# Performance work log

Measured on AMD Instinct MI355X. Metric: run time of the kernel, lower is better.

## Reference

```python
import jax, jax.numpy as jnp
import numpy as np

N_NODES, BATCH, VOCAB, HID, OUT = 2047, 128, 32, 128, 128


def setup_inputs() -> dict:
    key = jax.random.key(0)
    ks = jax.random.split(key, 18)
    w = 0.05  # small init scale (xavier-ish for these sizes)
    rn = lambda k, s, sc=w: jax.random.normal(k, s, dtype=jnp.float32) * sc
    return {
        "targets": jax.random.normal(ks[0], (N_NODES, BATCH, VOCAB), dtype=jnp.float32),
        "masks": jnp.ones((N_NODES, BATCH), dtype=jnp.float32),
        "wir_w": rn(ks[1], (HID, VOCAB)), "wir_b": rn(ks[2], (HID,)),
        "whr_w": rn(ks[3], (HID, 2 * HID)), "whr_b": rn(ks[4], (HID,)),
        "wiz_w": rn(ks[5], (HID, VOCAB)), "wiz_b": rn(ks[6], (HID,)),
        "whz_w": rn(ks[7], (HID, 2 * HID)), "whz_b": rn(ks[8], (HID,)),
        "win_w": rn(ks[9], (HID, VOCAB)), "win_b": rn(ks[10], (HID,)),
        "whn_w": rn(ks[11], (HID, 2 * HID)), "whn_b": rn(ks[12], (HID,)),
        "mu_w": rn(ks[13], (OUT, HID)), "mu_b": rn(ks[14], (OUT,)),
        "lv_w": rn(ks[15], (OUT, HID)), "lv_b": rn(ks[16], (OUT,)),
    }


def _encode(targets, masks, wir_w, wir_b, whr_w, whr_b, wiz_w, wiz_b,
            whz_w, whz_b, win_w, win_b, whn_w, whn_b):
    # Complete binary tree in heap layout: level d occupies nodes [2^d-1, 2^(d+1)-1).
    # Bottom-up level sweep == the original node-by-node recursion, but each
    # level's GRU221 cells are batched into one fused GEMM group.
    Nn, B, V = targets.shape
    H = wir_w.shape[0]
    D = int(np.log2(Nn + 1))  # static at trace time
    h_prev = None  # hidden states of the level below, [2^(d+1)*B, H]
    for d in range(D - 1, -1, -1):
        n = 1 << d
        start = n - 1
        x = targets[start:start + n].reshape(n * B, V)
        m = masks[start:start + n].reshape(n * B, 1)
        if h_prev is None:  # leaves: zero children
            h1 = jnp.zeros((n * B, H), dtype=targets.dtype)
            h2 = h1
        else:
            hp = h_prev.reshape(2 * n, B, H)
            h1 = hp[0::2].reshape(n * B, H)  # left children (heap idx 2i+1)
            h2 = hp[1::2].reshape(n * B, H)  # right children (heap idx 2i+2)
        h = jnp.concatenate([h1, h2], axis=1)  # [nB, 2H]
        r = jax.nn.sigmoid(x @ wir_w.T + wir_b + h @ whr_w.T + whr_b)
        z = jax.nn.sigmoid(x @ wiz_w.T + wiz_b + h @ whz_w.T + whz_b)
        c = jnp.tanh(x @ win_w.T + win_b + r * (h @ whn_w.T + whn_b))
        h_out = (1 - z) * c + z * 0.5 * h1 + z * 0.5 * h2
        h_prev = h_out * m
    return h_prev  # root hidden, [B, H]


def reference(targets, masks, wir_w, wir_b, whr_w, whr_b, wiz_w, wiz_b,
              whz_w, whz_b, win_w, win_b, whn_w, whn_b,
              mu_w, mu_b, lv_w, lv_b):
    root = _encode(targets, masks, wir_w, wir_b, whr_w, whr_b,
                   wiz_w, wiz_b, whz_w, whz_b, win_w, win_b, whn_w, whn_b)
    mu = root @ mu_w.T + mu_b
    logvar = root @ lv_w.T + lv_b
    return mu, logvar
```

## Files before the change

kernel.cpp:

```cpp
#include <hip/hip_runtime.h>
#include <hip/hip_bf16.h>
#include <math.h>

#define B 128
#define V 32
#define H 128
#define LDH 264
#define NTHR 256

typedef __attribute__((ext_vector_type(8))) short bf16x8;
typedef __attribute__((ext_vector_type(4))) float f32x4;

__device__ inline f32x4 mfma_wx(bf16x8 wf, bf16x8 xf, f32x4 c) {
    return __builtin_amdgcn_mfma_f32_16x16x32_bf16(wf, xf, c, 0, 0, 0);
}
__device__ inline unsigned short f2bf(float f) {
    __hip_bfloat16 h = __float2bfloat16(f);
    return __builtin_bit_cast(unsigned short, h);
}
__device__ inline float bf2f(unsigned short u) {
    unsigned int x = ((unsigned int)u) << 16;
    return __builtin_bit_cast(float, x);
}
__device__ inline float sig_pre(float y) {
    return __builtin_amdgcn_rcpf(1.f + __builtin_amdgcn_exp2f(y));
}
__device__ inline float tanh_pre(float y) {
    return 1.f - 2.f * __builtin_amdgcn_rcpf(__builtin_amdgcn_exp2f(y) + 1.f);
}
__device__ inline bf16x8 load_xfrag(const float* p) {
    float4 a = *(const float4*)p;
    float4 b = *(const float4*)(p + 4);
    bf16x8 r;
    r[0] = (short)f2bf(a.x); r[1] = (short)f2bf(a.y);
    r[2] = (short)f2bf(a.z); r[3] = (short)f2bf(a.w);
    r[4] = (short)f2bf(b.x); r[5] = (short)f2bf(b.y);
    r[6] = (short)f2bf(b.z); r[7] = (short)f2bf(b.w);
    return r;
}
__device__ inline uint2 pack4(float a, float b, float c, float d) {
    uint2 r;
    r.x = (unsigned int)f2bf(a) | ((unsigned int)f2bf(b) << 16);
    r.y = (unsigned int)f2bf(c) | ((unsigned int)f2bf(d) << 16);
    return r;
}

__global__ void prep_pack(const float* __restrict__ wir_w, const float* __restrict__ whr_w,
                          const float* __restrict__ wiz_w, const float* __restrict__ whz_w,
                          const float* __restrict__ win_w, const float* __restrict__ whn_w,
                          const float* __restrict__ wir_b, const float* __restrict__ whr_b,
                          const float* __restrict__ wiz_b, const float* __restrict__ whz_b,
                          const float* __restrict__ win_b, const float* __restrict__ whn_b,
                          const float* __restrict__ mu_w, const float* __restrict__ mu_b,
                          const float* __restrict__ lv_w, const float* __restrict__ lv_b,
                          unsigned short* __restrict__ wFrag, unsigned short* __restrict__ pFrag,
                          float* __restrict__ bias)
{
    int idx = blockIdx.x * blockDim.x + threadIdx.x;
    if (idx < 13824) {
        int lane = idx & 63;
        int ctks = idx >> 6;
        int ct = ctks % 24;
        int ks = ctks / 24;
        int g = ct >> 3;
        int t = ct & 7;
        int u = t * 16 + (lane & 15);
        const float scl = (g == 2) ? 2.88539008f : -1.44269504f;
        const float* wi = (g == 0) ? wir_w : (g == 1) ? wiz_w : win_w;
        const float* wh = (g == 0) ? whr_w : (g == 1) ? whz_w : whn_w;
        unsigned short v[8] __attribute__((aligned(16)));
        #pragma unroll
        for (int i = 0; i < 8; ++i) {
            float f;
            if (ks == 0) { int k = 8 * (lane >> 4) + i; f = wi[u * V + k]; }
            else         { int k = (ks - 1) * 32 + 8 * (lane >> 4) + i; f = wh[u * 256 + k]; }
            v[i] = f2bf(f * scl);
        }
        *(int4*)(wFrag + (size_t)idx * 8) = *(const int4*)v;
    } else if (idx < 13824 + 4096) {
        int pidx = idx - 13824;
        int lane = pidx & 63;
        int rest = pidx >> 6;
        int ct2 = rest & 15;
        int ks = rest >> 4;
        int sel = ct2 >> 3, tl = ct2 & 7;
        int u = tl * 16 + (lane & 15);
        const float* wsrc = sel ? lv_w : mu_w;
        unsigned short v[8] __attribute__((aligned(16)));
        #pragma unroll
        for (int i = 0; i < 8; ++i) {
            int k = ks * 32 + 8 * (lane >> 4) + i;
            v[i] = f2bf(wsrc[u * H + k]);
        }
        *(int4*)(pFrag + (size_t)pidx * 8) = *(const int4*)v;
    }
    if (idx < 6 * H) {
        int s = idx / H, u = idx % H;
        float val;
        if (s == 0)      val = (wir_b[u] + whr_b[u]) * -1.44269504f;
        else if (s == 1) val = (wiz_b[u] + whz_b[u]) * -1.44269504f;
        else if (s == 2) val = win_b[u] * 2.88539008f;
        else if (s == 3) val = whn_b[u] * 2.88539008f;
        else if (s == 4) val = mu_b[u];
        else             val = lv_b[u];
        bias[idx] = val;
    }
}

__global__ __launch_bounds__(NTHR, 4) void leaf_d9_kernel(
    const float* __restrict__ targets, const float* __restrict__ masks,
    unsigned short* __restrict__ lvl9,
    const unsigned short* __restrict__ wFrag, const float* __restrict__ bias)
{
    __shared__ __attribute__((aligned(16))) unsigned short h_lds[32 * LDH];

    const int tid = threadIdx.x;
    const int lane = tid & 63;
    const int w = tid >> 6;
    const int l15 = lane & 15;
    const int lg = lane >> 4;
    const int j = blockIdx.x >> 2;
    const int q = blockIdx.x & 3;

    bf16x8 w0[2][3];
    #pragma unroll
    for (int t = 0; t < 2; ++t)
        #pragma unroll
        for (int g = 0; g < 3; ++g)
            w0[t][g] = *(const bf16x8*)(wFrag + (((size_t)g * 8 + 2 * w + t) * 64 + lane) * 8);

    f32x4 b_r[2], b_z[2], b_in[2], b_hn[2];
    #pragma unroll
    for (int t = 0; t < 2; ++t) {
        int u0 = w * 32 + t * 16 + lg * 4;
        b_r[t]  = *(const f32x4*)(bias + u0);
        b_z[t]  = *(const f32x4*)(bias + 128 + u0);
        b_in[t] = *(const f32x4*)(bias + 256 + u0);
        b_hn[t] = *(const f32x4*)(bias + 384 + u0);
    }

    const size_t r9 = (size_t)(511 + j) * B + (size_t)q * 32;
    bf16x8 x9_0 = load_xfrag(targets + (r9 + l15) * V + 8 * lg);
    bf16x8 x9_1 = load_xfrag(targets + (r9 + 16 + l15) * V + 8 * lg);

    #pragma unroll
    for (int c = 0; c < 2; ++c) {
        const size_t crow = (size_t)(1023 + 2 * j + c) * B + (size_t)q * 32;
        bf16x8 xf0 = load_xfrag(targets + (crow + l15) * V + 8 * lg);
        bf16x8 xf1 = load_xfrag(targets + (crow + 16 + l15) * V + 8 * lg);
        f32x4 ar[2][2], az[2][2], an[2][2];
        #pragma unroll
        for (int t = 0; t < 2; ++t) {
            ar[0][t] = b_r[t];  ar[1][t] = b_r[t];
            az[0][t] = b_z[t];  az[1][t] = b_z[t];
            an[0][t] = b_in[t]; an[1][t] = b_in[t];
        }
        #pragma unroll
        for (int t = 0; t < 2; ++t) {
            ar[0][t] = mfma_wx(w0[t][0], xf0, ar[0][t]);
            ar[1][t] = mfma_wx(w0[t][0], xf1, ar[1][t]);
            az[0][t] = mfma_wx(w0[t][1], xf0, az[0][t]);
            az[1][t] = mfma_wx(w0[t][1], xf1, az[1][t]);
            an[0][t] = mfma_wx(w0[t][2], xf0, an[0][t]);
            an[1][t] = mfma_wx(w0[t][2], xf1, an[1][t]);
        }
        #pragma unroll
        for (int rt = 0; rt < 2; ++rt) {
            int row = rt * 16 + l15;
            float m = masks[crow + row];
            #pragma unroll
            for (int t = 0; t < 2; ++t) {
                int u0 = w * 32 + t * 16 + lg * 4;
                float ho[4];
                #pragma unroll
                for (int reg = 0; reg < 4; ++reg) {
                    float rg = sig_pre(ar[rt][t][reg]);
                    float zg = sig_pre(az[rt][t][reg]);
                    float cg = tanh_pre(an[rt][t][reg] + rg * b_hn[t][reg]);
                    ho[reg] = (cg - zg * cg) * m;
                }
                *(uint2*)(&h_lds[row * LDH + c * 128 + u0]) = pack4(ho[0], ho[1], ho[2], ho[3]);
            }
        }
    }
    __syncthreads();

    f32x4 acc_r[2][2], acc_z[2][2], acc_in[2][2], acc_hn[2][2];
    #pragma unroll
    for (int t = 0; t < 2; ++t) {
        acc_r[0][t] = b_r[t];   acc_r[1][t] = b_r[t];
        acc_z[0][t] = b_z[t];   acc_z[1][t] = b_z[t];
        acc_in[0][t] = b_in[t]; acc_in[1][t] = b_in[t];
        acc_hn[0][t] = b_hn[t]; acc_hn[1][t] = b_hn[t];
    }
    #pragma unroll
    for (int t = 0; t < 2; ++t) {
        acc_r[0][t] = mfma_wx(w0[t][0], x9_0, acc_r[0][t]);
        acc_r[1][t] = mfma_wx(w0[t][0], x9_1, acc_r[1][t]);
        acc_z[0][t] = mfma_wx(w0[t][1], x9_0, acc_z[0][t]);
        acc_z[1][t] = mfma_wx(w0[t][1], x9_1, acc_z[1][t]);
        acc_in[0][t] = mfma_wx(w0[t][2], x9_0, acc_in[0][t]);
        acc_in[1][t] = mfma_wx(w0[t][2], x9_1, acc_in[1][t]);
    }
    #pragma unroll 2
    for (int ks = 1; ks <= 8; ++ks) {
        bf16x8 a0 = *(const bf16x8*)(&h_lds[l15 * LDH + (ks - 1) * 32 + 8 * lg]);
        bf16x8 a1 = *(const bf16x8*)(&h_lds[(16 + l15) * LDH + (ks - 1) * 32 + 8 * lg]);
        size_t fb = (size_t)ks * 24 * 64;
        #pragma unroll
        for (int t = 0; t < 2; ++t) {
            int tt = 2 * w + t;
            bf16x8 wr_ = *(const bf16x8*)(wFrag + (fb + (size_t)(tt) * 64 + lane) * 8);
            bf16x8 wz_ = *(const bf16x8*)(wFrag + (fb + (size_t)(8 + tt) * 64 + lane) * 8);
            bf16x8 wn_ = *(const bf16x8*)(wFrag + (fb + (size_t)(16 + tt) * 64 + lane) * 8);
            acc_r[0][t] = mfma_wx(wr_, a0, acc_r[0][t]);
            acc_r[1][t] = mfma_wx(wr_, a1, acc_r[1][t]);
            acc_z[0][t] = mfma_wx(wz_, a0, acc_z[0][t]);
            acc_z[1][t] = mfma_wx(wz_, a1, acc_z[1][t]);
            acc_hn[0][t] = mfma_wx(wn_, a0, acc_hn[0][t]);
            acc_hn[1][t] = mfma_wx(wn_, a1, acc_hn[1][t]);
        }
    }
    #pragma unroll
    for (int rt = 0; rt < 2; ++rt) {
        int row = rt * 16 + l15;
        float m = masks[r9 + row];
        #pragma unroll
        for (int t = 0; t < 2; ++t) {
            int u0 = w * 32 + t * 16 + lg * 4;
            ushort4 h1v = *(const ushort4*)(&h_lds[row * LDH + u0]);
            ushort4 h2v = *(const ushort4*)(&h_lds[row * LDH + 128 + u0]);
            const unsigned short* h1p = (const unsigned short*)&h1v;
            const unsigned short* h2p = (const unsigned short*)&h2v;
            float ho[4];
            #pragma unroll
            for (int reg = 0; reg < 4; ++reg) {
                float rg = sig_pre(acc_r[rt][t][reg]);
                float zg = sig_pre(acc_z[rt][t][reg]);
                float cg = tanh_pre(acc_in[rt][t][reg] + rg * acc_hn[rt][t][reg]);
                float hm = 0.5f * bf2f(h1p[reg]) + 0.5f * bf2f(h2p[reg]);
                ho[reg] = (cg + zg * (hm - cg)) * m;
            }
            *(uint2*)(lvl9 + ((size_t)j * B + (size_t)q * 32 + row) * H + u0) =
                pack4(ho[0], ho[1], ho[2], ho[3]);
        }
    }
}

__global__ __launch_bounds__(NTHR, 4) void level_kernel(
    const float* __restrict__ targets, const float* __restrict__ masks,
    int start,
    const unsigned short* __restrict__ prev, unsigned short* __restrict__ outb,
    const unsigned short* __restrict__ wFrag, const float* __restrict__ bias)
{
    __shared__ __attribute__((aligned(16))) unsigned short h_lds[32 * LDH];

    const int tid = threadIdx.x;
    const int lane = tid & 63;
    const int w = tid >> 6;
    const int l15 = lane & 15;
    const int lg = lane >> 4;
    const int n = blockIdx.x >> 2;
    const int q = blockIdx.x & 3;

    #pragma unroll
    for (int t = 0; t < 4; ++t) {
        int task = t * NTHR + tid;
        int row = task >> 5;
        int ck = task & 31;
        int4 v = *(const int4*)(prev + (((size_t)(2 * n + (ck >> 4))) * B + (size_t)q * 32 + row) * H + (ck & 15) * 8);
        *(int4*)(&h_lds[row * LDH + ck * 8]) = v;
    }
    const size_t rx = (size_t)(start + n) * B + (size_t)q * 32;
    bf16x8 x0 = load_xfrag(targets + (rx + l15) * V + 8 * lg);
    bf16x8 x1 = load_xfrag(targets + (rx + 16 + l15) * V + 8 * lg);

    f32x4 b_r[2], b_z[2], b_in[2], b_hn[2];
    #pragma unroll
    for (int t = 0; t < 2; ++t) {
        int u0 = w * 32 + t * 16 + lg * 4;
        b_r[t]  = *(const f32x4*)(bias + u0);
        b_z[t]  = *(const f32x4*)(bias + 128 + u0);
        b_in[t] = *(const f32x4*)(bias + 256 + u0);
        b_hn[t] = *(const f32x4*)(bias + 384 + u0);
    }
    __syncthreads();

    f32x4 acc_r[2][2], acc_z[2][2], acc_in[2][2], acc_hn[2][2];
    #pragma unroll
    for (int t = 0; t < 2; ++t) {
        acc_r[0][t] = b_r[t];   acc_r[1][t] = b_r[t];
        acc_z[0][t] = b_z[t];   acc_z[1][t] = b_z[t];
        acc_in[0][t] = b_in[t]; acc_in[1][t] = b_in[t];
        acc_hn[0][t] = b_hn[t]; acc_hn[1][t] = b_hn[t];
    }
    #pragma unroll
    for (int t = 0; t < 2; ++t) {
        int tt = 2 * w + t;
        bf16x8 wr_ = *(const bf16x8*)(wFrag + ((size_t)(tt) * 64 + lane) * 8);
        bf16x8 wz_ = *(const bf16x8*)(wFrag + ((size_t)(8 + tt) * 64 + lane) * 8);
        bf16x8 wn_ = *(const bf16x8*)(wFrag + ((size_t)(16 + tt) * 64 + lane) * 8);
        acc_r[0][t] = mfma_wx(wr_, x0, acc_r[0][t]);
        acc_r[1][t] = mfma_wx(wr_, x1, acc_r[1][t]);
        acc_z[0][t] = mfma_wx(wz_, x0, acc_z[0][t]);
        acc_z[1][t] = mfma_wx(wz_, x1, acc_z[1][t]);
        acc_in[0][t] = mfma_wx(wn_, x0, acc_in[0][t]);
        acc_in[1][t] = mfma_wx(wn_, x1, acc_in[1][t]);
    }
    #pragma unroll 2
    for (int ks = 1; ks <= 8; ++ks) {
        bf16x8 a0 = *(const bf16x8*)(&h_lds[l15 * LDH + (ks - 1) * 32 + 8 * lg]);
        bf16x8 a1 = *(const bf16x8*)(&h_lds[(16 + l15) * LDH + (ks - 1) * 32 + 8 * lg]);
        size_t fb = (size_t)ks * 24 * 64;
        #pragma unroll
        for (int t = 0; t < 2; ++t) {
            int tt = 2 * w + t;
            bf16x8 wr_ = *(const bf16x8*)(wFrag + (fb + (size_t)(tt) * 64 + lane) * 8);
            bf16x8 wz_ = *(const bf16x8*)(wFrag + (fb + (size_t)(8 + tt) * 64 + lane) * 8);
            bf16x8 wn_ = *(const bf16x8*)(wFrag + (fb + (size_t)(16 + tt) * 64 + lane) * 8);
            acc_r[0][t] = mfma_wx(wr_, a0, acc_r[0][t]);
            acc_r[1][t] = mfma_wx(wr_, a1, acc_r[1][t]);
            acc_z[0][t] = mfma_wx(wz_, a0, acc_z[0][t]);
            acc_z[1][t] = mfma_wx(wz_, a1, acc_z[1][t]);
            acc_hn[0][t] = mfma_wx(wn_, a0, acc_hn[0][t]);
            acc_hn[1][t] = mfma_wx(wn_, a1, acc_hn[1][t]);
        }
    }
    #pragma unroll
    for (int rt = 0; rt < 2; ++rt) {
        int row = rt * 16 + l15;
        float m = masks[rx + row];
        #pragma unroll
        for (int t = 0; t < 2; ++t) {
            int u0 = w * 32 + t * 16 + lg * 4;
            ushort4 h1v = *(const ushort4*)(&h_lds[row * LDH + u0]);
            ushort4 h2v = *(const ushort4*)(&h_lds[row * LDH + 128 + u0]);
            const unsigned short* h1p = (const unsigned short*)&h1v;
            const unsigned short* h2p = (const unsigned short*)&h2v;
            float ho[4];
            #pragma unroll
            for (int reg = 0; reg < 4; ++reg) {
                float rg = sig_pre(acc_r[rt][t][reg]);
                float zg = sig_pre(acc_z[rt][t][reg]);
                float cg = tanh_pre(acc_in[rt][t][reg] + rg * acc_hn[rt][t][reg]);
                float hm = 0.5f * bf2f(h1p[reg]) + 0.5f * bf2f(h2p[reg]);
                ho[reg] = (cg + zg * (hm - cg)) * m;
            }
            *(uint2*)(outb + ((size_t)n * B + (size_t)q * 32 + row) * H + u0) =
                pack4(ho[0], ho[1], ho[2], ho[3]);
        }
    }
}

__global__ __launch_bounds__(NTHR, 4) void pair_kernel(
    const float* __restrict__ targets, const float* __restrict__ masks,
    int du,
    const unsigned short* __restrict__ prev,
    unsigned short* __restrict__ outl,
    const unsigned short* __restrict__ wFrag, const float* __restrict__ bias,
    int do_proj, const unsigned short* __restrict__ pFrag, float* __restrict__ proj_out)
{
    __shared__ __attribute__((aligned(16))) unsigned short hc[32 * LDH];
    __shared__ __attribute__((aligned(16))) unsigned short hp[16 * LDH];

    const int tid = threadIdx.x;
    const int lane = tid & 63;
    const int w = tid >> 6;
    const int l15 = lane & 15;
    const int lg = lane >> 4;
    const int p = blockIdx.x >> 3;
    const int c8 = blockIdx.x & 7;
    const int dl = du - 1;

    #pragma unroll
    for (int t = 0; t < 4; ++t) {
        int task = t * NTHR + tid;
        int row = task >> 5;
        int ck = task & 31;
        int gnode = 4 * p + ((row >> 4) << 1) + (ck >> 4);
        int4 v = *(const int4*)(prev + (((size_t)gnode) * B + (size_t)c8 * 16 + (row & 15)) * H + (ck & 15) * 8);
        *(int4*)(&hc[row * LDH + ck * 8]) = v;
    }
    const size_t cbase = (size_t)((1 << du) - 1) + 2 * p;
    bf16x8 xc0 = load_xfrag(targets + ((cbase) * B + (size_t)c8 * 16 + l15) * V + 8 * lg);
    bf16x8 xc1 = load_xfrag(targets + ((cbase + 1) * B + (size_t)c8 * 16 + l15) * V + 8 * lg);
    const size_t pnode = (size_t)((1 << dl) - 1) + p;
    bf16x8 xp = load_xfrag(targets + (pnode * B + (size_t)c8 * 16 + l15) * V + 8 * lg);

    f32x4 b_r[2], b_z[2], b_in[2], b_hn[2];
    #pragma unroll
    for (int t = 0; t < 2; ++t) {
        int u0 = w * 32 + t * 16 + lg * 4;
        b_r[t]  = *(const f32x4*)(bias + u0);
        b_z[t]  = *(const f32x4*)(bias + 128 + u0);
        b_in[t] = *(const f32x4*)(bias + 256 + u0);
        b_hn[t] = *(const f32x4*)(bias + 384 + u0);
    }
    __syncthreads();

    {
        f32x4 acc_r[2][2], acc_z[2][2], acc_in[2][2], acc_hn[2][2];
        #pragma unroll
        for (int t = 0; t < 2; ++t) {
            acc_r[0][t] = b_r[t];   acc_r[1][t] = b_r[t];
            acc_z[0][t] = b_z[t];   acc_z[1][t] = b_z[t];
            acc_in[0][t] = b_in[t]; acc_in[1][t] = b_in[t];
            acc_hn[0][t] = b_hn[t]; acc_hn[1][t] = b_hn[t];
        }
        #pragma unroll
        for (int t = 0; t < 2; ++t) {
            int tt = 2 * w + t;
            bf16x8 wr_ = *(const bf16x8*)(wFrag + ((size_t)(tt) * 64 + lane) * 8);
            bf16x8 wz_ = *(const bf16x8*)(wFrag + ((size_t)(8 + tt) * 64 + lane) * 8);
            bf16x8 wn_ = *(const bf16x8*)(wFrag + ((size_t)(16 + tt) * 64 + lane) * 8);
            acc_r[0][t] = mfma_wx(wr_, xc0, acc_r[0][t]);
            acc_r[1][t] = mfma_wx(wr_, xc1, acc_r[1][t]);
            acc_z[0][t] = mfma_wx(wz_, xc0, acc_z[0][t]);
            acc_z[1][t] = mfma_wx(wz_, xc1, acc_z[1][t]);
            acc_in[0][t] = mfma_wx(wn_, xc0, acc_in[0][t]);
            acc_in[1][t] = mfma_wx(wn_, xc1, acc_in[1][t]);
        }
        #pragma unroll 2
        for (int ks = 1; ks <= 8; ++ks) {
            bf16x8 a0 = *(const bf16x8*)(&hc[l15 * LDH + (ks - 1) * 32 + 8 * lg]);
            bf16x8 a1 = *(const bf16x8*)(&hc[(16 + l15) * LDH + (ks - 1) * 32 + 8 * lg]);
            size_t fb = (size_t)ks * 24 * 64;
            #pragma unroll
            for (int t = 0; t < 2; ++t) {
                int tt = 2 * w + t;
                bf16x8 wr_ = *(const bf16x8*)(wFrag + (fb + (size_t)(tt) * 64 + lane) * 8);
                bf16x8 wz_ = *(const bf16x8*)(wFrag + (fb + (size_t)(8 + tt) * 64 + lane) * 8);
                bf16x8 wn_ = *(const bf16x8*)(wFrag + (fb + (size_t)(16 + tt) * 64 + lane) * 8);
                acc_r[0][t] = mfma_wx(wr_, a0, acc_r[0][t]);
                acc_r[1][t] = mfma_wx(wr_, a1, acc_r[1][t]);
                acc_z[0][t] = mfma_wx(wz_, a0, acc_z[0][t]);
                acc_z[1][t] = mfma_wx(wz_, a1, acc_z[1][t]);
                acc_hn[0][t] = mfma_wx(wn_, a0, acc_hn[0][t]);
                acc_hn[1][t] = mfma_wx(wn_, a1, acc_hn[1][t]);
            }
        }
        #pragma unroll
        for (int rt = 0; rt < 2; ++rt) {
            float m = masks[(cbase + rt) * B + (size_t)c8 * 16 + l15];
            int hrow = rt * 16 + l15;
            #pragma unroll
            for (int t = 0; t < 2; ++t) {
                int u0 = w * 32 + t * 16 + lg * 4;
                ushort4 h1v = *(const ushort4*)(&hc[hrow * LDH + u0]);
                ushort4 h2v = *(const ushort4*)(&hc[hrow * LDH + 128 + u0]);
                const unsigned short* h1p = (const unsigned short*)&h1v;
                const unsigned short* h2p = (const unsigned short*)&h2v;
                float ho[4];
                #pragma unroll
                for (int reg = 0; reg < 4; ++reg) {
                    float rg = sig_pre(acc_r[rt][t][reg]);
                    float zg = sig_pre(acc_z[rt][t][reg]);
                    float cg = tanh_pre(acc_in[rt][t][reg] + rg * acc_hn[rt][t][reg]);
                    float hm = 0.5f * bf2f(h1p[reg]) + 0.5f * bf2f(h2p[reg]);
                    ho[reg] = (cg + zg * (hm - cg)) * m;
                }
                *(uint2*)(&hp[l15 * LDH + rt * 128 + u0]) = pack4(ho[0], ho[1], ho[2], ho[3]);
            }
        }
    }
    __syncthreads();

    {
        f32x4 acc_r[2], acc_z[2], acc_in[2], acc_hn[2];
        #pragma unroll
        for (int t = 0; t < 2; ++t) {
            acc_r[t] = b_r[t]; acc_z[t] = b_z[t]; acc_in[t] = b_in[t]; acc_hn[t] = b_hn[t];
        }
        #pragma unroll
        for (int t = 0; t < 2; ++t) {
            int tt = 2 * w + t;
            bf16x8 wr_ = *(const bf16x8*)(wFrag + ((size_t)(tt) * 64 + lane) * 8);
            bf16x8 wz_ = *(const bf16x8*)(wFrag + ((size_t)(8 + tt) * 64 + lane) * 8);
            bf16x8 wn_ = *(const bf16x8*)(wFrag + ((size_t)(16 + tt) * 64 + lane) * 8);
            acc_r[t] = mfma_wx(wr_, xp, acc_r[t]);
            acc_z[t] = mfma_wx(wz_, xp, acc_z[t]);
            acc_in[t] = mfma_wx(wn_, xp, acc_in[t]);
        }
        #pragma unroll 2
        for (int ks = 1; ks <= 8; ++ks) {
            bf16x8 a = *(const bf16x8*)(&hp[l15 * LDH + (ks - 1) * 32 + 8 * lg]);
            size_t fb = (size_t)ks * 24 * 64;
            #pragma unroll
            for (int t = 0; t < 2; ++t) {
                int tt = 2 * w + t;
                bf16x8 wr_ = *(const bf16x8*)(wFrag + (fb + (size_t)(tt) * 64 + lane) * 8);
                bf16x8 wz_ = *(const bf16x8*)(wFrag + (fb + (size_t)(8 + tt) * 64 + lane) * 8);
                bf16x8 wn_ = *(const bf16x8*)(wFrag + (fb + (size_t)(16 + tt) * 64 + lane) * 8);
                acc_r[t] = mfma_wx(wr_, a, acc_r[t]);
                acc_z[t] = mfma_wx(wz_, a, acc_z[t]);
                acc_hn[t] = mfma_wx(wn_, a, acc_hn[t]);
            }
        }
        float m = masks[pnode * B + (size_t)c8 * 16 + l15];
        #pragma unroll
        for (int t = 0; t < 2; ++t) {
            int u0 = w * 32 + t * 16 + lg * 4;
            ushort4 h1v = *(const ushort4*)(&hp[l15 * LDH + u0]);
            ushort4 h2v = *(const ushort4*)(&hp[l15 * LDH + 128 + u0]);
            const unsigned short* h1p = (const unsigned short*)&h1v;
            const unsigned short* h2p = (const unsigned short*)&h2v;
            float ho[4];
            #pragma unroll
            for (int reg = 0; reg < 4; ++reg) {
                float rg = sig_pre(acc_r[t][reg]);
                float zg = sig_pre(acc_z[t][reg]);
                float cg = tanh_pre(acc_in[t][reg] + rg * acc_hn[t][reg]);
                float hm = 0.5f * bf2f(h1p[reg]) + 0.5f * bf2f(h2p[reg]);
                ho[reg] = (cg + zg * (hm - cg)) * m;
            }
            uint2 pk = pack4(ho[0], ho[1], ho[2], ho[3]);
            *(uint2*)(outl + ((size_t)p * B + (size_t)c8 * 16 + l15) * H + u0) = pk;
            if (do_proj) *(uint2*)(&hp[l15 * LDH + u0]) = pk;
        }
    }

    if (do_proj) {
        __syncthreads();
        f32x4 pa[4];
        #pragma unroll
        for (int jj = 0; jj < 4; ++jj) {
            int ct2 = 4 * w + jj;
            int sel = ct2 >> 3, tl = ct2 & 7;
            pa[jj] = *(const f32x4*)(bias + 512 + sel * 128 + tl * 16 + lg * 4);
        }
        #pragma unroll
        for (int ks = 0; ks < 4; ++ks) {
            bf16x8 a = *(const bf16x8*)(&hp[l15 * LDH + ks * 32 + 8 * lg]);
            #pragma unroll
            for (int jj = 0; jj < 4; ++jj) {
                bf16x8 f = *(const bf16x8*)(pFrag + (((size_t)ks * 16 + 4 * w + jj) * 64 + lane) * 8);
                pa[jj] = mfma_wx(f, a, pa[jj]);
            }
        }
        #pragma unroll
        for (int jj = 0; jj < 4; ++jj) {
            int ct2 = 4 * w + jj;
            int sel = ct2 >> 3, tl = ct2 & 7;
            int u0 = tl * 16 + lg * 4;
            int row = c8 * 16 + l15;
            *(f32x4*)(proj_out + ((size_t)sel * B + row) * H + u0) = pa[jj];
        }
    }
}

extern "C" void kernel_launch(void* const* d_in, const int* in_sizes, int n_in,
                              void* d_out, int out_size, void* d_ws, size_t ws_size,
                              hipStream_t stream)
{
    const float* targets = (const float*)d_in[0];
    const float* masks   = (const float*)d_in[1];
    const float* wir_w = (const float*)d_in[2];  const float* wir_b = (const float*)d_in[3];
    const float* whr_w = (const float*)d_in[4];  const float* whr_b = (const float*)d_in[5];
    const float* wiz_w = (const float*)d_in[6];  const float* wiz_b = (const float*)d_in[7];
    const float* whz_w = (const float*)d_in[8];  const float* whz_b = (const float*)d_in[9];
    const float* win_w = (const float*)d_in[10]; const float* win_b = (const float*)d_in[11];
    const float* whn_w = (const float*)d_in[12]; const float* whn_b = (const float*)d_in[13];
    const float* mu_w  = (const float*)d_in[14]; const float* mu_b  = (const float*)d_in[15];
    const float* lv_w  = (const float*)d_in[16]; const float* lv_b  = (const float*)d_in[17];

    unsigned short* ws16 = (unsigned short*)d_ws;
    unsigned short* lvl9 = ws16;
    unsigned short* lvl8 = lvl9 + (size_t)512 * B * H;
    unsigned short* lvl6 = lvl8 + (size_t)256 * B * H;
    unsigned short* lvl4 = lvl6 + (size_t)64 * B * H;
    unsigned short* lvl2 = lvl4 + (size_t)16 * B * H;
    unsigned short* lvl0 = lvl2 + (size_t)4 * B * H;
    unsigned short* wFrag = lvl0 + (size_t)1 * B * H;
    unsigned short* pFrag = wFrag + 110592;
    float*          biasw = (float*)(pFrag + 32768);

    prep_pack<<<70, 256, 0, stream>>>(
        wir_w, whr_w, wiz_w, whz_w, win_w, whn_w,
        wir_b, whr_b, wiz_b, whz_b, win_b, whn_b,
        mu_w, mu_b, lv_w, lv_b, wFrag, pFrag, biasw);

    leaf_d9_kernel<<<2048, NTHR, 0, stream>>>(targets, masks, lvl9, wFrag, biasw);

    level_kernel<<<1024, NTHR, 0, stream>>>(targets, masks, 255, lvl9, lvl8, wFrag, biasw);

    pair_kernel<<<512, NTHR, 0, stream>>>(targets, masks, 7, lvl8, lvl6, wFrag, biasw,
                                          0, nullptr, nullptr);
    pair_kernel<<<128, NTHR, 0, stream>>>(targets, masks, 5, lvl6, lvl4, wFrag, biasw,
                                          0, nullptr, nullptr);
    pair_kernel<<<32, NTHR, 0, stream>>>(targets, masks, 3, lvl4, lvl2, wFrag, biasw,
                                         0, nullptr, nullptr);
    pair_kernel<<<8, NTHR, 0, stream>>>(targets, masks, 1, lvl2, lvl0, wFrag, biasw,
                                        1, pFrag, (float*)d_out);
}
```

Before: 136.1 us.

## Fuse leaf, level-9 and level-8 GRU cells into one subtree kernel

Merges the leaf/level-9 kernel and the level-8 kernel into a single kernel in which each block computes two level-9 nodes (each from its two leaf children) and then their level-8 parent. Level-9 hidden states stay in a second LDS buffer instead of going through global memory, which removes one launch and the write and reread of the level-9 activations. In exchange there are half as many blocks, each doing serialized work with extra barriers, and the larger LDS footprint may cut occupancy.

New measurement: 178.8 us. +31.3%, slower.

```diff
diff --git a/kernel.cpp b/kernel.cpp
--- a/kernel.cpp
+++ b/kernel.cpp
@@ -22,12 +22,8 @@
     unsigned int x = ((unsigned int)u) << 16;
     return __builtin_bit_cast(float, x);
 }
-__device__ inline float sig_pre(float y) {
-    return __builtin_amdgcn_rcpf(1.f + __builtin_amdgcn_exp2f(y));
-}
-__device__ inline float tanh_pre(float y) {
-    return 1.f - 2.f * __builtin_amdgcn_rcpf(__builtin_amdgcn_exp2f(y) + 1.f);
-}
+__device__ inline float sig_pre(float y)  { return __builtin_amdgcn_rcpf(1.f + __builtin_amdgcn_exp2f(y)); }
+__device__ inline float tanh_pre(float y) { return 1.f - 2.f * __builtin_amdgcn_rcpf(__builtin_amdgcn_exp2f(y) + 1.f); }
 __device__ inline bf16x8 load_xfrag(const float* p) {
     float4 a = *(const float4*)p;
     float4 b = *(const float4*)(p + 4);
@@ -107,19 +103,20 @@
     }
 }
 
-__global__ __launch_bounds__(NTHR, 4) void leaf_d9_kernel(
+__global__ __launch_bounds__(NTHR, 4) void subtree8_kernel(
     const float* __restrict__ targets, const float* __restrict__ masks,
-    unsigned short* __restrict__ lvl9,
+    unsigned short* __restrict__ lvl8,
     const unsigned short* __restrict__ wFrag, const float* __restrict__ bias)
 {
     __shared__ __attribute__((aligned(16))) unsigned short h_lds[32 * LDH];
+    __shared__ __attribute__((aligned(16))) unsigned short h2_lds[32 * LDH];
 
     const int tid = threadIdx.x;
     const int lane = tid & 63;
     const int w = tid >> 6;
     const int l15 = lane & 15;
     const int lg = lane >> 4;
-    const int j = blockIdx.x >> 2;
+    const int n = blockIdx.x >> 2;
     const int q = blockIdx.x & 3;
 
     bf16x8 w0[2][3];
@@ -139,215 +136,191 @@
         b_hn[t] = *(const f32x4*)(bias + 384 + u0);
     }
 
-    const size_t r9 = (size_t)(511 + j) * B + (size_t)q * 32;
-    bf16x8 x9_0 = load_xfrag(targets + (r9 + l15) * V + 8 * lg);
-    bf16x8 x9_1 = load_xfrag(targets + (r9 + 16 + l15) * V + 8 * lg);
-
-    #pragma unroll
-    for (int c = 0; c < 2; ++c) {
-        const size_t crow = (size_t)(1023 + 2 * j + c) * B + (size_t)q * 32;
-        bf16x8 xf0 = load_xfrag(targets + (crow + l15) * V + 8 * lg);
-        bf16x8 xf1 = load_xfrag(targets + (crow + 16 + l15) * V + 8 * lg);
-        f32x4 ar[2][2], az[2][2], an[2][2];
-        #pragma unroll
-        for (int t = 0; t < 2; ++t) {
-            ar[0][t] = b_r[t];  ar[1][t] = b_r[t];
-            az[0][t] = b_z[t];  az[1][t] = b_z[t];
-            an[0][t] = b_in[t]; an[1][t] = b_in[t];
-        }
-        #pragma unroll
-        for (int t = 0; t < 2; ++t) {
-            ar[0][t] = mfma_wx(w0[t][0], xf0, ar[0][t]);
-            ar[1][t] = mfma_wx(w0[t][0], xf1, ar[1][t]);
-            az[0][t] = mfma_wx(w0[t][1], xf0, az[0][t]);
-            az[1][t] = mfma_wx(w0[t][1], xf1, az[1][t]);
-            an[0][t] = mfma_wx(w0[t][2], xf0, an[0][t]);
-            an[1][t] = mfma_wx(w0[t][2], xf1, an[1][t]);
-        }
+    const size_t r8 = (size_t)(255 + n) * B + (size_t)q * 32;
+    bf16x8 x8_0 = load_xfrag(targets + (r8 + l15) * V + 8 * lg);
+    bf16x8 x8_1 = load_xfrag(targets + (r8 + 16 + l15) * V + 8 * lg);
+
+    for (int half = 0; half < 2; ++half) {
+        const int j = 2 * n + half;
+        const size_t r9 = (size_t)(511 + j) * B + (size_t)q * 32;
+        bf16x8 x9_0 = load_xfrag(targets + (r9 + l15) * V + 8 * lg);
+        bf16x8 x9_1 = load_xfrag(targets + (r9 + 16 + l15) * V + 8 * lg);
+
+        #pragma unroll
+        for (int c = 0; c < 2; ++c) {
+            const size_t crow = (size_t)(1023 + 2 * j + c) * B + (size_t)q * 32;
+            bf16x8 xf0 = load_xfrag(targets + (crow + l15) * V + 8 * lg);
+            bf16x8 xf1 = load_xfrag(targets + (crow + 16 + l15) * V + 8 * lg);
+            f32x4 ar[2][2], az[2][2], an[2][2];
+            #pragma unroll
+            for (int t = 0; t < 2; ++t) {
+                ar[0][t] = b_r[t];  ar[1][t] = b_r[t];
+                az[0][t] = b_z[t];  az[1][t] = b_z[t];
+                an[0][t] = b_in[t]; an[1][t] = b_in[t];
+            }
+            #pragma unroll
+            for (int t = 0; t < 2; ++t) {
+                ar[0][t] = mfma_wx(w0[t][0], xf0, ar[0][t]);
+                ar[1][t] = mfma_wx(w0[t][0], xf1, ar[1][t]);
+                az[0][t] = mfma_wx(w0[t][1], xf0, az[0][t]);
+                az[1][t] = mfma_wx(w0[t][1], xf1, az[1][t]);
+                an[0][t] = mfma_wx(w0[t][2], xf0, an[0][t]);
+                an[1][t] = mfma_wx(w0[t][2], xf1, an[1][t]);
+            }
+            #pragma unroll
+            for (int rt = 0; rt < 2; ++rt) {
+                int row = rt * 16 + l15;
+                float m = masks[crow + row];
+                #pragma unroll
+                for (int t = 0; t < 2; ++t) {
+                    int u0 = w * 32 + t * 16 + lg * 4;
+                    float ho[4];
+                    #pragma unroll
+                    for (int reg = 0; reg < 4; ++reg) {
+                        float rg = sig_pre(ar[rt][t][reg]);
+                        float zg = sig_pre(az[rt][t][reg]);
+                        float cg = tanh_pre(an[rt][t][reg] + rg * b_hn[t][reg]);
+                        ho[reg] = (cg - zg * cg) * m;
+                    }
+                    *(uint2*)(&h_lds[row * LDH + c * 128 + u0]) = pack4(ho[0], ho[1], ho[2], ho[3]);
+                }
+            }
+        }
+        __syncthreads();
+
+        f32x4 acc_r[2][2], acc_z[2][2], acc_in[2][2], acc_hn[2][2];
+        #pragma unroll
+        for (int t = 0; t < 2; ++t) {
+            acc_r[0][t] = b_r[t];   acc_r[1][t] = b_r[t];
+            acc_z[0][t] = b_z[t];   acc_z[1][t] = b_z[t];
+            acc_in[0][t] = b_in[t]; acc_in[1][t] = b_in[t];
+            acc_hn[0][t] = b_hn[t]; acc_hn[1][t] = b_hn[t];
+        }
+        #pragma unroll
+        for (int t = 0; t < 2; ++t) {
+            acc_r[0][t] = mfma_wx(w0[t][0], x9_0, acc_r[0][t]);
+            acc_r[1][t] = mfma_wx(w0[t][0], x9_1, acc_r[1][t]);
+            acc_z[0][t] = mfma_wx(w0[t][1], x9_0, acc_z[0][t]);
+            acc_z[1][t] = mfma_wx(w0[t][1], x9_1, acc_z[1][t]);
+            acc_in[0][t] = mfma_wx(w0[t][2], x9_0, acc_in[0][t]);
+            acc_in[1][t] = mfma_wx(w0[t][2], x9_1, acc_in[1][t]);
+        }
+        #pragma unroll 2
+        for (int ks = 1; ks <= 8; ++ks) {
+            bf16x8 a0 = *(const bf16x8*)(&h_lds[l15 * LDH + (ks - 1) * 32 + 8 * lg]);
+            bf16x8 a1 = *(const bf16x8*)(&h_lds[(16 + l15) * LDH + (ks - 1) * 32 + 8 * lg]);
+            size_t fb = (size_t)ks * 24 * 64;
+            #pragma unroll
+            for (int t = 0; t < 2; ++t) {
+                int tt = 2 * w + t;
+                bf16x8 wr_ = *(const bf16x8*)(wFrag + (fb + (size_t)(tt) * 64 + lane) * 8);
+                bf16x8 wz_ = *(const bf16x8*)(wFrag + (fb + (size_t)(8 + tt) * 64 + lane) * 8);
+                bf16x8 wn_ = *(const bf16x8*)(wFrag + (fb + (size_t)(16 + tt) * 64 + lane) * 8);
+                acc_r[0][t] = mfma_wx(wr_, a0, acc_r[0][t]);
+                acc_r[1][t] = mfma_wx(wr_, a1, acc_r[1][t]);
+                acc_z[0][t] = mfma_wx(wz_, a0, acc_z[0][t]);
+                acc_z[1][t] = mfma_wx(wz_, a1, acc_z[1][t]);
+                acc_hn[0][t] = mfma_wx(wn_, a0, acc_hn[0][t]);
+                acc_hn[1][t] = mfma_wx(wn_, a1, acc_hn[1][t]);
+            }
+        }
+        ushort4 h1v[2][2], h2v[2][2];
         #pragma unroll
         for (int rt = 0; rt < 2; ++rt) {
             int row = rt * 16 + l15;
-            float m = masks[crow + row];
             #pragma unroll
             for (int t = 0; t < 2; ++t) {
                 int u0 = w * 32 + t * 16 + lg * 4;
+                h1v[rt][t] = *(const ushort4*)(&h_lds[row * LDH + u0]);
+                h2v[rt][t] = *(const ushort4*)(&h_lds[row * LDH + 128 + u0]);
+            }
+        }
+        __syncthreads();
+
+        #pragma unroll
+        for (int rt = 0; rt < 2; ++rt) {
+            int row = rt * 16 + l15;
+            float m = masks[r9 + row];
+            #pragma unroll
+            for (int t = 0; t < 2; ++t) {
+                int u0 = w * 32 + t * 16 + lg * 4;
+                const unsigned short* h1p = (const unsigned short*)&h1v[rt][t];
+                const unsigned short* h2p = (const unsigned short*)&h2v[rt][t];
                 float ho[4];
                 #pragma unroll
                 for (int reg = 0; reg < 4; ++reg) {
-                    float rg = sig_pre(ar[rt][t][reg]);
-                    float zg = sig_pre(az[rt][t][reg]);
-                    float cg = tanh_pre(an[rt][t][reg] + rg * b_hn[t][reg]);
-                    ho[reg] = (cg - zg * cg) * m;
+                    float rg = sig_pre(acc_r[rt][t][reg]);
+                    float zg = sig_pre(acc_z[rt][t][reg]);
+                    float cg = tanh_pre(acc_in[rt][t][reg] + rg * acc_hn[rt][t][reg]);
+                    float hm = 0.5f * bf2f(h1p[reg]) + 0.5f * bf2f(h2p[reg]);
+                    ho[reg] = (cg + zg * (hm - cg)) * m;
                 }
-                *(uint2*)(&h_lds[row * LDH + c * 128 + u0]) = pack4(ho[0], ho[1], ho[2], ho[3]);
+                *(uint2*)(&h2_lds[row * LDH + half * 128 + u0]) = pack4(ho[0], ho[1], ho[2], ho[3]);
             }
         }
     }
     __syncthreads();
 
-    f32x4 acc_r[2][2], acc_z[2][2], acc_in[2][2], acc_hn[2][2];
-    #pragma unroll
-    for (int t = 0; t < 2; ++t) {
-        acc_r[0][t] = b_r[t];   acc_r[1][t] = b_r[t];
-        acc_z[0][t] = b_z[t];   acc_z[1][t] = b_z[t];
-        acc_in[0][t] = b_in[t]; acc_in[1][t] = b_in[t];
-        acc_hn[0][t] = b_hn[t]; acc_hn[1][t] = b_hn[t];
-    }
-    #pragma unroll
-    for (int t = 0; t < 2; ++t) {
-        acc_r[0][t] = mfma_wx(w0[t][0], x9_0, acc_r[0][t]);
-        acc_r[1][t] = mfma_wx(w0[t][0], x9_1, acc_r[1][t]);
-        acc_z[0][t] = mfma_wx(w0[t][1], x9_0, acc_z[0][t]);
-        acc_z[1][t] = mfma_wx(w0[t][1], x9_1, acc_z[1][t]);
-        acc_in[0][t] = mfma_wx(w0[t][2], x9_0, acc_in[0][t]);
-        acc_in[1][t] = mfma_wx(w0[t][2], x9_1, acc_in[1][t]);
-    }
-    #pragma unroll 2
-    for (int ks = 1; ks <= 8; ++ks) {
-        bf16x8 a0 = *(const bf16x8*)(&h_lds[l15 * LDH + (ks - 1) * 32 + 8 * lg]);
-        bf16x8 a1 = *(const bf16x8*)(&h_lds[(16 + l15) * LDH + (ks - 1) * 32 + 8 * lg]);
-        size_t fb = (size_t)ks * 24 * 64;
-        #pragma unroll
-        for (int t = 0; t < 2; ++t) {
-            int tt = 2 * w + t;
-            bf16x8 wr_ = *(const bf16x8*)(wFrag + (fb + (size_t)(tt) * 64 + lane) * 8);
-            bf16x8 wz_ = *(const bf16x8*)(wFrag + (fb + (size_t)(8 + tt) * 64 + lane) * 8);
-            bf16x8 wn_ = *(const bf16x8*)(wFrag + (fb + (size_t)(16 + tt) * 64 + lane) * 8);
-            acc_r[0][t] = mfma_wx(wr_, a0, acc_r[0][t]);
-            acc_r[1][t] = mfma_wx(wr_, a1, acc_r[1][t]);
-            acc_z[0][t] = mfma_wx(wz_, a0, acc_z[0][t]);
-            acc_z[1][t] = mfma_wx(wz_, a1, acc_z[1][t]);
-            acc_hn[0][t] = mfma_wx(wn_, a0, acc_hn[0][t]);
-            acc_hn[1][t] = mfma_wx(wn_, a1, acc_hn[1][t]);
-        }
-    }
-    #pragma unroll
-    for (int rt = 0; rt < 2; ++rt) {
-        int row = rt * 16 + l15;
-        float m = masks[r9 + row];
-        #pragma unroll
-        for (int t = 0; t < 2; ++t) {
-            int u0 = w * 32 + t * 16 + lg * 4;
-            ushort4 h1v = *(const ushort4*)(&h_lds[row * LDH + u0]);
-            ushort4 h2v = *(const ushort4*)(&h_lds[row * LDH + 128 + u0]);
-            const unsigned short* h1p = (const unsigned short*)&h1v;
-            const unsigned short* h2p = (const unsigned short*)&h2v;
-            float ho[4];
-            #pragma unroll
-            for (int reg = 0; reg < 4; ++reg) {
-                float rg = sig_pre(acc_r[rt][t][reg]);
-                float zg = sig_pre(acc_z[rt][t][reg]);
-                float cg = tanh_pre(acc_in[rt][t][reg] + rg * acc_hn[rt][t][reg]);
-                float hm = 0.5f * bf2f(h1p[reg]) + 0.5f * bf2f(h2p[reg]);
-                ho[reg] = (cg + zg * (hm - cg)) * m;
-            }
-            *(uint2*)(lvl9 + ((size_t)j * B + (size_t)q * 32 + row) * H + u0) =
-                pack4(ho[0], ho[1], ho[2], ho[3]);
-        }
-    }
-}
-
-__global__ __launch_bounds__(NTHR, 4) void level_kernel(
-    const float* __restrict__ targets, const float* __restrict__ masks,
-    int start,
-    const unsigned short* __restrict__ prev, unsigned short* __restrict__ outb,
-    const unsigned short* __restrict__ wFrag, const float* __restrict__ bias)
-{
-    __shared__ __attribute__((aligned(16))) unsigned short h_lds[32 * LDH];
-
-    const int tid = threadIdx.x;
-    const int lane = tid & 63;
-    const int w = tid >> 6;
-    const int l15 = lane & 15;
-    const int lg = lane >> 4;
-    const int n = blockIdx.x >> 2;
-    const int q = blockIdx.x & 3;
-
-    #pragma unroll
-    for (int t = 0; t < 4; ++t) {
-        int task = t * NTHR + tid;
-        int row = task >> 5;
-        int ck = task & 31;
-        int4 v = *(const int4*)(prev + (((size_t)(2 * n + (ck >> 4))) * B + (size_t)q * 32 + row) * H + (ck & 15) * 8);
-        *(int4*)(&h_lds[row * LDH + ck * 8]) = v;
-    }
-    const size_t rx = (size_t)(start + n) * B + (size_t)q * 32;
-    bf16x8 x0 = load_xfrag(targets + (rx + l15) * V + 8 * lg);
-    bf16x8 x1 = load_xfrag(targets + (rx + 16 + l15) * V + 8 * lg);
-
-    f32x4 b_r[2], b_z[2], b_in[2], b_hn[2];
-    #pragma unroll
-    for (int t = 0; t < 2; ++t) {
-        int u0 = w * 32 + t * 16 + lg * 4;
-        b_r[t]  = *(const f32x4*)(bias + u0);
-        b_z[t]  = *(const f32x4*)(bias + 128 + u0);
-        b_in[t] = *(const f32x4*)(bias + 256 + u0);
-        b_hn[t] = *(const f32x4*)(bias + 384 + u0);
-    }
-    __syncthreads();
-
-    f32x4 acc_r[2][2], acc_z[2][2], acc_in[2][2], acc_hn[2][2];
-    #pragma unroll
-    for (int t = 0; t < 2; ++t) {
-        acc_r[0][t] = b_r[t];   acc_r[1][t] = b_r[t];
-        acc_z[0][t] = b_z[t];   acc_z[1][t] = b_z[t];
-        acc_in[0][t] = b_in[t]; acc_in[1][t] = b_in[t];
-        acc_hn[0][t] = b_hn[t]; acc_hn[1][t] = b_hn[t];
-    }
-    #pragma unroll
-    for (int t = 0; t < 2; ++t) {
-        int tt = 2 * w + t;
-        bf16x8 wr_ = *(const bf16x8*)(wFrag + ((size_t)(tt) * 64 + lane) * 8);
-        bf16x8 wz_ = *(const bf16x8*)(wFrag + ((size_t)(8 + tt) * 64 + lane) * 8);
-        bf16x8 wn_ = *(const bf16x8*)(wFrag + ((size_t)(16 + tt) * 64 + lane) * 8);
-        acc_r[0][t] = mfma_wx(wr_, x0, acc_r[0][t]);
-        acc_r[1][t] = mfma_wx(wr_, x1, acc_r[1][t]);
-        acc_z[0][t] = mfma_wx(wz_, x0, acc_z[0][t]);
-        acc_z[1][t] = mfma_wx(wz_, x1, acc_z[1][t]);
-        acc_in[0][t] = mfma_wx(wn_, x0, acc_in[0][t]);
-        acc_in[1][t] = mfma_wx(wn_, x1, acc_in[1][t]);
-    }
-    #pragma unroll 2
-    for (int ks = 1; ks <= 8; ++ks) {
-        bf16x8 a0 = *(const bf16x8*)(&h_lds[l15 * LDH + (ks - 1) * 32 + 8 * lg]);
-        bf16x8 a1 = *(const bf16x8*)(&h_lds[(16 + l15) * LDH + (ks - 1) * 32 + 8 * lg]);
-        size_t fb = (size_t)ks * 24 * 64;
-        #pragma unroll
-        for (int t = 0; t < 2; ++t) {
-            int tt = 2 * w + t;
-            bf16x8 wr_ = *(const bf16x8*)(wFrag + (fb + (size_t)(tt) * 64 + lane) * 8);
-            bf16x8 wz_ = *(const bf16x8*)(wFrag + (fb + (size_t)(8 + tt) * 64 + lane) * 8);
-            bf16x8 wn_ = *(const bf16x8*)(wFrag + (fb + (size_t)(16 + tt) * 64 + lane) * 8);
-            acc_r[0][t] = mfma_wx(wr_, a0, acc_r[0][t]);
-            acc_r[1][t] = mfma_wx(wr_, a1, acc_r[1][t]);
-            acc_z[0][t] = mfma_wx(wz_, a0, acc_z[0][t]);
-            acc_z[1][t] = mfma_wx(wz_, a1, acc_z[1][t]);
-            acc_hn[0][t] = mfma_wx(wn_, a0, acc_hn[0][t]);
-            acc_hn[1][t] = mfma_wx(wn_, a1, acc_hn[1][t]);
-        }
-    }
-    #pragma unroll
-    for (int rt = 0; rt < 2; ++rt) {
-        int row = rt * 16 + l15;
-        float m = masks[rx + row];
-        #pragma unroll
-        for (int t = 0; t < 2; ++t) {
-            int u0 = w * 32 + t * 16 + lg * 4;
-            ushort4 h1v = *(const ushort4*)(&h_lds[row * LDH + u0]);
-            ushort4 h2v = *(const ushort4*)(&h_lds[row * LDH + 128 + u0]);
-            const unsigned short* h1p = (const unsigned short*)&h1v;
-            const unsigned short* h2p = (const unsigned short*)&h2v;
-            float ho[4];
-            #pragma unroll
-            for (int reg = 0; reg < 4; ++reg) {
-                float rg = sig_pre(acc_r[rt][t][reg]);
-                float zg = sig_pre(acc_z[rt][t][reg]);
-                float cg = tanh_pre(acc_in[rt][t][reg] + rg * acc_hn[rt][t][reg]);
-                float hm = 0.5f * bf2f(h1p[reg]) + 0.5f * bf2f(h2p[reg]);
-                ho[reg] = (cg + zg * (hm - cg)) * m;
-            }
-            *(uint2*)(outb + ((size_t)n * B + (size_t)q * 32 + row) * H + u0) =
-                pack4(ho[0], ho[1], ho[2], ho[3]);
+    {
+        f32x4 acc_r[2][2], acc_z[2][2], acc_in[2][2], acc_hn[2][2];
+        #pragma unroll
+        for (int t = 0; t < 2; ++t) {
+            acc_r[0][t] = b_r[t];   acc_r[1][t] = b_r[t];
+            acc_z[0][t] = b_z[t];   acc_z[1][t] = b_z[t];
+            acc_in[0][t] = b_in[t]; acc_in[1][t] = b_in[t];
+            acc_hn[0][t] = b_hn[t]; acc_hn[1][t] = b_hn[t];
+        }
+        #pragma unroll
+        for (int t = 0; t < 2; ++t) {
+            acc_r[0][t] = mfma_wx(w0[t][0], x8_0, acc_r[0][t]);
+            acc_r[1][t] = mfma_wx(w0[t][0], x8_1, acc_r[1][t]);
+            acc_z[0][t] = mfma_wx(w0[t][1], x8_0, acc_z[0][t]);
+            acc_z[1][t] = mfma_wx(w0[t][1], x8_1, acc_z[1][t]);
+            acc_in[0][t] = mfma_wx(w0[t][2], x8_0, acc_in[0][t]);
+            acc_in[1][t] = mfma_wx(w0[t][2], x8_1, acc_in[1][t]);
+        }
+        #pragma unroll 2
+        for (int ks = 1; ks <= 8; ++ks) {
+            bf16x8 a0 = *(const bf16x8*)(&h2_lds[l15 * LDH + (ks - 1) * 32 + 8 * lg]);
+            bf16x8 a1 = *(const bf16x8*)(&h2_lds[(16 + l15) * LDH + (ks - 1) * 32 + 8 * lg]);
+            size_t fb = (size_t)ks * 24 * 64;
+            #pragma unroll
+            for (int t = 0; t < 2; ++t) {
+                int tt = 2 * w + t;
+                bf16x8 wr_ = *(const bf16x8*)(wFrag + (fb + (size_t)(tt) * 64 + lane) * 8);
+                bf16x8 wz_ = *(const bf16x8*)(wFrag + (fb + (size_t)(8 + tt) * 64 + lane) * 8);
+                bf16x8 wn_ = *(const bf16x8*)(wFrag + (fb + (size_t)(16 + tt) * 64 + lane) * 8);
+                acc_r[0][t] = mfma_wx(wr_, a0, acc_r[0][t]);
+                acc_r[1][t] = mfma_wx(wr_, a1, acc_r[1][t]);
+                acc_z[0][t] = mfma_wx(wz_, a0, acc_z[0][t]);
+                acc_z[1][t] = mfma_wx(wz_, a1, acc_z[1][t]);
+                acc_hn[0][t] = mfma_wx(wn_, a0, acc_hn[0][t]);
+                acc_hn[1][t] = mfma_wx(wn_, a1, acc_hn[1][t]);
+            }
+        }
+        #pragma unroll
+        for (int rt = 0; rt < 2; ++rt) {
+            int row = rt * 16 + l15;
+            float m = masks[r8 + row];
+            #pragma unroll
+            for (int t = 0; t < 2; ++t) {
+                int u0 = w * 32 + t * 16 + lg * 4;
+                ushort4 h1v = *(const ushort4*)(&h2_lds[row * LDH + u0]);
+                ushort4 h2v = *(const ushort4*)(&h2_lds[row * LDH + 128 + u0]);
+                const unsigned short* h1p = (const unsigned short*)&h1v;
+                const unsigned short* h2p = (const unsigned short*)&h2v;
+                float ho[4];
+                #pragma unroll
+                for (int reg = 0; reg < 4; ++reg) {
+                    float rg = sig_pre(acc_r[rt][t][reg]);
+                    float zg = sig_pre(acc_z[rt][t][reg]);
+                    float cg = tanh_pre(acc_in[rt][t][reg] + rg * acc_hn[rt][t][reg]);
+                    float hm = 0.5f * bf2f(h1p[reg]) + 0.5f * bf2f(h2p[reg]);
+                    ho[reg] = (cg + zg * (hm - cg)) * m;
+                }
+                *(uint2*)(lvl8 + ((size_t)n * B + (size_t)q * 32 + row) * H + u0) =
+                    pack4(ho[0], ho[1], ho[2], ho[3]);
+            }
         }
     }
 }
@@ -564,8 +537,7 @@
     const float* lv_w  = (const float*)d_in[16]; const float* lv_b  = (const float*)d_in[17];
 
     unsigned short* ws16 = (unsigned short*)d_ws;
-    unsigned short* lvl9 = ws16;
-    unsigned short* lvl8 = lvl9 + (size_t)512 * B * H;
+    unsigned short* lvl8 = ws16;
     unsigned short* lvl6 = lvl8 + (size_t)256 * B * H;
     unsigned short* lvl4 = lvl6 + (size_t)64 * B * H;
     unsigned short* lvl2 = lvl4 + (size_t)16 * B * H;
@@ -579,9 +551,7 @@
         wir_b, whr_b, wiz_b, whz_b, win_b, whn_b,
         mu_w, mu_b, lv_w, lv_b, wFrag, pFrag, biasw);
 
-    leaf_d9_kernel<<<2048, NTHR, 0, stream>>>(targets, masks, lvl9, wFrag, biasw);
-
-    level_kernel<<<1024, NTHR, 0, stream>>>(targets, masks, 255, lvl9, lvl8, wFrag, biasw);
+    subtree8_kernel<<<1024, NTHR, 0, stream>>>(targets, masks, lvl8, wFrag, biasw);
 
     pair_kernel<<<512, NTHR, 0, stream>>>(targets, masks, 7, lvl8, lvl6, wFrag, biasw,
                                           0, nullptr, nullptr);
```
